# Kernel tuning notes

Measured on AMD Instinct MI355X. Metric: run time of the kernel, lower is better.

## Reference

```python
import jax, jax.numpy as jnp
import numpy as np

NEG_SLOPE = 0.2

def gat_conv(x, src, dst, n_nodes, W, a_src, a_dst, bias, heads, out_c):
    # x: [N, in]; W: [in, heads*out_c]; a_src/a_dst: [heads, out_c]; bias: [heads*out_c]
    h = (x @ W).reshape(n_nodes, heads, out_c)            # [N,H,C]
    e_s = jnp.sum(h * a_src, axis=-1)                     # [N,H] per-node src score
    e_d = jnp.sum(h * a_dst, axis=-1)                     # [N,H] per-node dst score
    e = jax.nn.leaky_relu(e_s[src] + e_d[dst], NEG_SLOPE) # [E,H]
    # segment softmax over destination neighborhoods
    emax = jax.ops.segment_max(e, dst, num_segments=n_nodes)  # [N,H]
    emax = jnp.where(jnp.isfinite(emax), emax, 0.0)
    p = jnp.exp(e - emax[dst])                            # [E,H]
    denom = jax.ops.segment_sum(p, dst, num_segments=n_nodes)  # [N,H]
    alpha = p / (denom[dst] + 1e-16)                      # [E,H]
    msg = h[src] * alpha[:, :, None]                      # [E,H,C]
    out = jax.ops.segment_sum(msg, dst, num_segments=n_nodes)  # [N,H,C]
    return out.reshape(n_nodes, heads * out_c) + bias


def setup_inputs() -> dict:
    key = jax.random.key(0)
    ks = jax.random.split(key, 10)
    N, E, IN, OUT, H = 50000, 1600000, 128, 32, 2
    x = jax.random.normal(ks[0], (N, IN), dtype=jnp.float32)
    edge_index = jax.random.randint(ks[1], (2, E), 0, N, dtype=jnp.int64)
    s = 0.1
    W1 = jax.random.normal(ks[2], (IN, H * OUT), dtype=jnp.float32) * s
    a_src1 = jax.random.normal(ks[3], (H, OUT), dtype=jnp.float32) * s
    a_dst1 = jax.random.normal(ks[4], (H, OUT), dtype=jnp.float32) * s
    b1 = jnp.zeros((H * OUT,), dtype=jnp.float32)
    W2 = jax.random.normal(ks[5], (H * OUT, OUT), dtype=jnp.float32) * s
    a_src2 = jax.random.normal(ks[6], (1, OUT), dtype=jnp.float32) * s
    a_dst2 = jax.random.normal(ks[7], (1, OUT), dtype=jnp.float32) * s
    b2 = jnp.zeros((OUT,), dtype=jnp.float32)
    return {"x": x, "edge_index": edge_index, "W1": W1, "a_src1": a_src1,
            "a_dst1": a_dst1, "b1": b1, "W2": W2, "a_src2": a_src2,
            "a_dst2": a_dst2, "b2": b2}


def reference(x, edge_index, W1, a_src1, a_dst1, b1, W2, a_src2, a_dst2, b2):
    N = x.shape[0]
    # add_self_loops=True (PyG GATConv default)
    loops = jnp.arange(N, dtype=edge_index.dtype)
    ei = jnp.concatenate([edge_index, jnp.stack([loops, loops])], axis=1)
    src, dst = ei[0], ei[1]
    h = gat_conv(x, src, dst, N, W1, a_src1, a_dst1, b1, heads=2, out_c=32)
    h = jax.nn.relu(h)
    out = gat_conv(h, src, dst, N, W2, a_src2, a_dst2, b2, heads=1, out_c=32)
    return out
```

## Files before the change

kernel.cpp:

```cpp
#include <hip/hip_runtime.h>
#include <hip/hip_fp16.h>

#define NEG_SLOPE 0.2f
#define DB 128
#define NB_MAX 512
#define EPB 4096
#define CAP 8192


__global__ __launch_bounds__(256) void k_part(const int* __restrict__ srcv,
                                              const int* __restrict__ dstv,
                                              int* __restrict__ gcur,
                                              int* __restrict__ ebuf, int E) {
  __shared__ int sh[NB_MAX];
  __shared__ int lbase[NB_MAX];
  int t = threadIdx.x;
  sh[t] = 0; sh[t + 256] = 0;
  __syncthreads();
  int base = blockIdx.x * EPB;
  int dd[16];
#pragma unroll
  for (int i = 0; i < 16; ++i) {
    int e = base + i * 256 + t;
    dd[i] = (e < E) ? dstv[e] : -1;
    if (dd[i] >= 0) atomicAdd(&sh[dd[i] >> 7], 1);
  }
  __syncthreads();
#pragma unroll
  for (int i = 0; i < 2; ++i) {
    int b = t + 256 * i;
    int c = sh[b];
    lbase[b] = c ? (b * CAP + atomicAdd(&gcur[b], c)) : 0;
    sh[b] = 0;
  }
  __syncthreads();
#pragma unroll
  for (int i = 0; i < 16; ++i) {
    if (dd[i] >= 0) {
      int e = base + i * 256 + t;
      int b = dd[i] >> 7;
      int r = atomicAdd(&sh[b], 1);
      ebuf[lbase[b] + r] = srcv[e] | ((dd[i] & 127) << 16);
    }
  }
}

__global__ __launch_bounds__(256) void k_csr(const int* __restrict__ gcur,
                                             const int* __restrict__ ebuf,
                                             int* __restrict__ rowbeg,
                                             int* __restrict__ rowend,
                                             int* __restrict__ col, int N) {
  int b = blockIdx.x;
  int cnt = gcur[b];
  int base = b * CAP;
  int dbase = b * DB;
  __shared__ int dh[DB];
  __shared__ int sc[DB];
  int t = threadIdx.x;
  if (t < DB) dh[t] = 0;
  __syncthreads();
  for (int j = t; j < cnt; j += 256) {
    int p = ebuf[base + j];
    atomicAdd(&dh[p >> 16], 1);
  }
  __syncthreads();
  int v = 0;
  if (t < DB) { v = dh[t]; sc[t] = v; }
  __syncthreads();
  for (int off = 1; off < DB; off <<= 1) {
    int u = 0;
    if (t < DB && t >= off) u = sc[t - off];
    __syncthreads();
    if (t < DB) sc[t] += u;
    __syncthreads();
  }
  if (t < DB) {
    int excl = sc[t] - v;
    int d = dbase + t;
    if (d < N) {
      rowbeg[d] = base + excl;
      rowend[d] = base + excl + v;
    }
    dh[t] = base + excl;
  }
  __syncthreads();
  for (int j = t; j < cnt; j += 256) {
    int p = ebuf[base + j];
    int r = atomicAdd(&dh[p >> 16], 1);
    col[r] = p & 0xFFFF;
  }
}

__global__ __launch_bounds__(256) void k_gemm1(const float* __restrict__ x,
                                               const float* __restrict__ W,
                                               const float* __restrict__ a_src,
                                               const float* __restrict__ a_dst,
                                               __half* __restrict__ h1,
                                               float* __restrict__ es,
                                               float* __restrict__ ed, int N) {
  __shared__ float sXT[128 * 64];
  __shared__ float sW[128 * 64];
  const int t = threadIdx.x;
  const int r0 = blockIdx.x * 64;

  {
    const float4* Wp = (const float4*)W;
    float4* sWp = (float4*)sW;
#pragma unroll
    for (int i = 0; i < 8; ++i) sWp[t + i * 256] = Wp[t + i * 256];
  }
  {
    int r = t & 63;
    int kq = t >> 6;
    int gr = r0 + r;
    bool ok = gr < N;
    const float* xr = x + (size_t)gr * 128;
#pragma unroll
    for (int p = 0; p < 8; ++p) {
      int k = (kq + p * 4) * 4;
      float4 v = ok ? *(const float4*)(xr + k) : make_float4(0.f, 0.f, 0.f, 0.f);
      sXT[(k + 0) * 64 + r] = v.x;
      sXT[(k + 1) * 64 + r] = v.y;
      sXT[(k + 2) * 64 + r] = v.z;
      sXT[(k + 3) * 64 + r] = v.w;
    }
  }
  __syncthreads();

  const int tx = t & 15, ty = t >> 4;
  float4 acc0 = make_float4(0.f, 0.f, 0.f, 0.f);
  float4 acc1 = acc0, acc2 = acc0, acc3 = acc0;
#pragma unroll 8
  for (int k = 0; k < 128; ++k) {
    float4 av = *(const float4*)(sXT + k * 64 + ty * 4);
    float4 bv = *(const float4*)(sW + k * 64 + tx * 4);
    acc0.x += av.x * bv.x; acc0.y += av.x * bv.y; acc0.z += av.x * bv.z; acc0.w += av.x * bv.w;
    acc1.x += av.y * bv.x; acc1.y += av.y * bv.y; acc1.z += av.y * bv.z; acc1.w += av.y * bv.w;
    acc2.x += av.z * bv.x; acc2.y += av.z * bv.y; acc2.z += av.z * bv.z; acc2.w += av.z * bv.w;
    acc3.x += av.w * bv.x; acc3.y += av.w * bv.y; acc3.z += av.w * bv.z; acc3.w += av.w * bv.w;
  }

  float4 accs[4] = {acc0, acc1, acc2, acc3};
#pragma unroll
  for (int i = 0; i < 4; ++i) {
    int gr = r0 + ty * 4 + i;
    if (gr < N) {
      union { __half2 h[2]; float2 f; } u;
      u.h[0] = __float22half2_rn(make_float2(accs[i].x, accs[i].y));
      u.h[1] = __float22half2_rn(make_float2(accs[i].z, accs[i].w));
      *(float2*)(h1 + (size_t)gr * 64 + tx * 4) = u.f;
    }
  }

  float4 asv = *(const float4*)(a_src + tx * 4);
  float4 adv = *(const float4*)(a_dst + tx * 4);
  float esp[4], edp[4];
#pragma unroll
  for (int i = 0; i < 4; ++i) {
    esp[i] = accs[i].x * asv.x + accs[i].y * asv.y + accs[i].z * asv.z + accs[i].w * asv.w;
    edp[i] = accs[i].x * adv.x + accs[i].y * adv.y + accs[i].z * adv.z + accs[i].w * adv.w;
  }
#pragma unroll
  for (int off = 1; off <= 4; off <<= 1) {
#pragma unroll
    for (int i = 0; i < 4; ++i) {
      esp[i] += __shfl_xor(esp[i], off);
      edp[i] += __shfl_xor(edp[i], off);
    }
  }
  if ((tx & 7) == 0) {
    int hh = tx >> 3;
#pragma unroll
    for (int i = 0; i < 4; ++i) {
      int gr = r0 + ty * 4 + i;
      if (gr < N) {
        es[gr * 2 + hh] = esp[i];
        ed[gr * 2 + hh] = edp[i];
      }
    }
  }
}

__global__ __launch_bounds__(256) void k_agg1(const int* __restrict__ rowbeg,
                                              const int* __restrict__ rowend,
                                              const int* __restrict__ col,
                                              const __half* __restrict__ h1,
                                              const float* __restrict__ es,
                                              const float* __restrict__ ed,
                                              const float* __restrict__ bias,
                                              float* __restrict__ out1, int N) {
  int d = (blockIdx.x * blockDim.x + threadIdx.x) >> 6;
  int lane = threadIdx.x & 63;
  if (d >= N) return;
  int g = lane >> 4;
  int q = lane & 15;
  int ch = q * 4;
  int hh = ch >> 5;
  float edv = ed[d * 2 + hh];

  float4 acc = make_float4(0.f, 0.f, 0.f, 0.f);
  float wsum = 0.f;

  if (g == 0) {
    float v = es[d * 2 + hh] + edv;
    v = v > 0.f ? v : NEG_SLOPE * v;
    float w = __expf(v);
    float2 raw = *(const float2*)(h1 + (size_t)d * 64 + ch);
    __half2* p2 = (__half2*)&raw;
    float2 lo = __half22float2(p2[0]);
    float2 hi = __half22float2(p2[1]);
    acc.x = w * lo.x; acc.y = w * lo.y; acc.z = w * hi.x; acc.w = w * hi.y;
    wsum = w;
  }

  int beg = rowbeg[d], end = rowend[d];
#pragma unroll 2
  for (int j = beg + g; j < end; j += 4) {
    int s = col[j];
    float vv = es[s * 2 + hh] + edv;
    vv = vv > 0.f ? vv : NEG_SLOPE * vv;
    float w = __expf(vv);
    float2 raw = *(const float2*)(h1 + (size_t)s * 64 + ch);
    __half2* p2 = (__half2*)&raw;
    float2 lo = __half22float2(p2[0]);
    float2 hi = __half22float2(p2[1]);
    acc.x += w * lo.x; acc.y += w * lo.y; acc.z += w * hi.x; acc.w += w * hi.y;
    wsum += w;
  }

#pragma unroll
  for (int off = 16; off <= 32; off <<= 1) {
    acc.x += __shfl_xor(acc.x, off);
    acc.y += __shfl_xor(acc.y, off);
    acc.z += __shfl_xor(acc.z, off);
    acc.w += __shfl_xor(acc.w, off);
    wsum  += __shfl_xor(wsum, off);
  }

  if (g == 0) {
    float inv = 1.f / (wsum + 1e-16f);
    const float4 bv = *(const float4*)(bias + ch);
    float4 o;
    o.x = acc.x * inv + bv.x;
    o.y = acc.y * inv + bv.y;
    o.z = acc.z * inv + bv.z;
    o.w = acc.w * inv + bv.w;
    *(float4*)(out1 + (size_t)d * 64 + ch) = o;
  }
}

__global__ __launch_bounds__(256) void k_gemm2(const float* __restrict__ out1,
                                               const float* __restrict__ W,
                                               const float* __restrict__ a_src,
                                               const float* __restrict__ a_dst,
                                               __half* __restrict__ hL2,
                                               float* __restrict__ es,
                                               float* __restrict__ ed, int N) {
  __shared__ float sXT[64 * 128];
  __shared__ float sW[64 * 32];
  const int t = threadIdx.x;
  const int r0 = blockIdx.x * 128;

  {
    const float4* Wp = (const float4*)W;
    float4* sWp = (float4*)sW;
#pragma unroll
    for (int i = 0; i < 2; ++i) sWp[t + i * 256] = Wp[t + i * 256];
  }
  {
    int r = t & 127;
    int kq = t >> 7;
    int gr = r0 + r;
    bool ok = gr < N;
    const float* xr = out1 + (size_t)gr * 64;
#pragma unroll
    for (int p = 0; p < 8; ++p) {
      int k = (kq + p * 2) * 4;
      float4 v = ok ? *(const float4*)(xr + k) : make_float4(0.f, 0.f, 0.f, 0.f);
      sXT[(k + 0) * 128 + r] = fmaxf(v.x, 0.f);
      sXT[(k + 1) * 128 + r] = fmaxf(v.y, 0.f);
      sXT[(k + 2) * 128 + r] = fmaxf(v.z, 0.f);
      sXT[(k + 3) * 128 + r] = fmaxf(v.w, 0.f);
    }
  }
  __syncthreads();

  const int tx = t & 7, ty = t >> 3;
  float4 acc0 = make_float4(0.f, 0.f, 0.f, 0.f);
  float4 acc1 = acc0, acc2 = acc0, acc3 = acc0;
#pragma unroll 8
  for (int k = 0; k < 64; ++k) {
    float4 av = *(const float4*)(sXT + k * 128 + ty * 4);
    float4 bv = *(const float4*)(sW + k * 32 + tx * 4);
    acc0.x += av.x * bv.x; acc0.y += av.x * bv.y; acc0.z += av.x * bv.z; acc0.w += av.x * bv.w;
    acc1.x += av.y * bv.x; acc1.y += av.y * bv.y; acc1.z += av.y * bv.z; acc1.w += av.y * bv.w;
    acc2.x += av.z * bv.x; acc2.y += av.z * bv.y; acc2.z += av.z * bv.z; acc2.w += av.z * bv.w;
    acc3.x += av.w * bv.x; acc3.y += av.w * bv.y; acc3.z += av.w * bv.z; acc3.w += av.w * bv.w;
  }

  float4 accs[4] = {acc0, acc1, acc2, acc3};
#pragma unroll
  for (int i = 0; i < 4; ++i) {
    int gr = r0 + ty * 4 + i;
    if (gr < N) {
      union { __half2 h[2]; float2 f; } u;
      u.h[0] = __float22half2_rn(make_float2(accs[i].x, accs[i].y));
      u.h[1] = __float22half2_rn(make_float2(accs[i].z, accs[i].w));
      *(float2*)(hL2 + (size_t)gr * 32 + tx * 4) = u.f;
    }
  }

  float4 asv = *(const float4*)(a_src + tx * 4);
  float4 adv = *(const float4*)(a_dst + tx * 4);
  float esp[4], edp[4];
#pragma unroll
  for (int i = 0; i < 4; ++i) {
    esp[i] = accs[i].x * asv.x + accs[i].y * asv.y + accs[i].z * asv.z + accs[i].w * asv.w;
    edp[i] = accs[i].x * adv.x + accs[i].y * adv.y + accs[i].z * adv.z + accs[i].w * adv.w;
  }
#pragma unroll
  for (int off = 1; off <= 4; off <<= 1) {
#pragma unroll
    for (int i = 0; i < 4; ++i) {
      esp[i] += __shfl_xor(esp[i], off);
      edp[i] += __shfl_xor(edp[i], off);
    }
  }
  if (tx == 0) {
#pragma unroll
    for (int i = 0; i < 4; ++i) {
      int gr = r0 + ty * 4 + i;
      if (gr < N) {
        es[gr] = esp[i];
        ed[gr] = edp[i];
      }
    }
  }
}

__global__ __launch_bounds__(256) void k_agg2(const int* __restrict__ rowbeg,
                                              const int* __restrict__ rowend,
                                              const int* __restrict__ col,
                                              const __half* __restrict__ hL2,
                                              const float* __restrict__ es,
                                              const float* __restrict__ ed,
                                              const float* __restrict__ bias,
                                              float* __restrict__ out, int N) {
  int d = (blockIdx.x * blockDim.x + threadIdx.x) >> 6;
  int lane = threadIdx.x & 63;
  if (d >= N) return;
  int g = lane >> 3;
  int q = lane & 7;
  int ch = q * 4;
  float edv = ed[d];

  float4 acc = make_float4(0.f, 0.f, 0.f, 0.f);
  float wsum = 0.f;

  if (g == 0) {
    float v = es[d] + edv;
    v = v > 0.f ? v : NEG_SLOPE * v;
    float w = __expf(v);
    float2 raw = *(const float2*)(hL2 + (size_t)d * 32 + ch);
    __half2* p2 = (__half2*)&raw;
    float2 lo = __half22float2(p2[0]);
    float2 hi = __half22float2(p2[1]);
    acc.x = w * lo.x; acc.y = w * lo.y; acc.z = w * hi.x; acc.w = w * hi.y;
    wsum = w;
  }

  int beg = rowbeg[d], end = rowend[d];
#pragma unroll 2
  for (int j = beg + g; j < end; j += 8) {
    int s = col[j];
    float vv = es[s] + edv;
    vv = vv > 0.f ? vv : NEG_SLOPE * vv;
    float w = __expf(vv);
    float2 raw = *(const float2*)(hL2 + (size_t)s * 32 + ch);
    __half2* p2 = (__half2*)&raw;
    float2 lo = __half22float2(p2[0]);
    float2 hi = __half22float2(p2[1]);
    acc.x += w * lo.x; acc.y += w * lo.y; acc.z += w * hi.x; acc.w += w * hi.y;
    wsum += w;
  }

#pragma unroll
  for (int off = 8; off <= 32; off <<= 1) {
    acc.x += __shfl_xor(acc.x, off);
    acc.y += __shfl_xor(acc.y, off);
    acc.z += __shfl_xor(acc.z, off);
    acc.w += __shfl_xor(acc.w, off);
    wsum  += __shfl_xor(wsum, off);
  }

  if (g == 0) {
    float inv = 1.f / (wsum + 1e-16f);
    const float4 bv = *(const float4*)(bias + ch);
    float4 o;
    o.x = acc.x * inv + bv.x;
    o.y = acc.y * inv + bv.y;
    o.z = acc.z * inv + bv.z;
    o.w = acc.w * inv + bv.w;
    *(float4*)(out + (size_t)d * 32 + ch) = o;
  }
}

extern "C" void kernel_launch(void* const* d_in, const int* in_sizes, int n_in,
                              void* d_out, int out_size, void* d_ws, size_t ws_size,
                              hipStream_t stream) {
  const float* x      = (const float*)d_in[0];
  const int*   ei     = (const int*)d_in[1];
  const float* W1     = (const float*)d_in[2];
  const float* a_src1 = (const float*)d_in[3];
  const float* a_dst1 = (const float*)d_in[4];
  const float* b1     = (const float*)d_in[5];
  const float* W2     = (const float*)d_in[6];
  const float* a_src2 = (const float*)d_in[7];
  const float* a_dst2 = (const float*)d_in[8];
  const float* b2     = (const float*)d_in[9];
  float* out = (float*)d_out;

  const int N = in_sizes[0] / 128;
  const int E = in_sizes[1] / 2;
  const int NB = (N + DB - 1) / DB;
  const int* srcv = ei;
  const int* dstv = ei + E;

  char* base = (char*)d_ws;
  size_t off = 0;
  auto carve = [&](size_t bytes) {
    void* p = base + off;
    off += (bytes + 15) & ~(size_t)15;
    return p;
  };
  __half* h1     = (__half*)carve((size_t)N * 64 * 2);
  float*  es1    = (float*)carve((size_t)N * 2 * 4);
  float*  ed1    = (float*)carve((size_t)N * 2 * 4);
  float*  out1   = (float*)carve((size_t)N * 64 * 4);
  __half* hL2    = (__half*)carve((size_t)N * 32 * 2);
  float*  es2    = (float*)carve((size_t)N * 4);
  float*  ed2    = (float*)carve((size_t)N * 4);
  int*    gcur   = (int*)carve((size_t)NB_MAX * 4);
  int*    rowbeg = (int*)carve((size_t)N * 4);
  int*    rowend = (int*)carve((size_t)N * 4);
  int*    col    = (int*)carve((size_t)NB * CAP * 4);
  int*    ebuf   = (int*)carve((size_t)NB * CAP * 4);

  const int pblocks = (E + EPB - 1) / EPB;

  hipMemsetAsync(gcur, 0, (size_t)NB_MAX * sizeof(int), stream);
  k_part<<<pblocks, 256, 0, stream>>>(srcv, dstv, gcur, ebuf, E);
  k_csr<<<NB, 256, 0, stream>>>(gcur, ebuf, rowbeg, rowend, col, N);

  k_gemm1<<<(N + 63) / 64, 256, 0, stream>>>(x, W1, a_src1, a_dst1, h1, es1, ed1, N);
  k_agg1<<<((size_t)N * 64 + 255) / 256, 256, 0, stream>>>(rowbeg, rowend, col, h1, es1, ed1, b1, out1, N);

  k_gemm2<<<(N + 127) / 128, 256, 0, stream>>>(out1, W2, a_src2, a_dst2, hL2, es2, ed2, N);
  k_agg2<<<((size_t)N * 64 + 255) / 256, 256, 0, stream>>>(rowbeg, rowend, col, hL2, es2, ed2, b2, out, N);
}
```

Before: 222.4 us.

## Merge GEMM1 with edge partition, use 16-bit CSR columns, widen aggregation loads

Folds the first-layer GEMM and the edge partition into one launch: the first G1 blocks do the GEMM and the rest partition edges, so the two independent jobs overlap and one launch is saved. The CSR column array becomes unsigned short, which halves the index traffic during aggregation. Both aggregation kernels now load 8 halves per lane (16-byte loads) with more edge groups per wavefront. The shared 64KB shared-memory block may lower occupancy for the partition blocks, and dropping the unroll pragma may reduce memory-level parallelism.

```diff
diff --git a/kernel.cpp b/kernel.cpp
--- a/kernel.cpp
+++ b/kernel.cpp
@@ -7,40 +7,125 @@
 #define EPB 4096
 #define CAP 8192
 
-
-__global__ __launch_bounds__(256) void k_part(const int* __restrict__ srcv,
-                                              const int* __restrict__ dstv,
-                                              int* __restrict__ gcur,
-                                              int* __restrict__ ebuf, int E) {
-  __shared__ int sh[NB_MAX];
-  __shared__ int lbase[NB_MAX];
-  int t = threadIdx.x;
-  sh[t] = 0; sh[t + 256] = 0;
-  __syncthreads();
-  int base = blockIdx.x * EPB;
-  int dd[16];
-#pragma unroll
-  for (int i = 0; i < 16; ++i) {
-    int e = base + i * 256 + t;
-    dd[i] = (e < E) ? dstv[e] : -1;
-    if (dd[i] >= 0) atomicAdd(&sh[dd[i] >> 7], 1);
-  }
-  __syncthreads();
-#pragma unroll
-  for (int i = 0; i < 2; ++i) {
-    int b = t + 256 * i;
-    int c = sh[b];
-    lbase[b] = c ? (b * CAP + atomicAdd(&gcur[b], c)) : 0;
-    sh[b] = 0;
-  }
-  __syncthreads();
-#pragma unroll
-  for (int i = 0; i < 16; ++i) {
-    if (dd[i] >= 0) {
+__global__ __launch_bounds__(256) void k_g1p(
+    const float* __restrict__ x, const float* __restrict__ W,
+    const float* __restrict__ a_src, const float* __restrict__ a_dst,
+    __half* __restrict__ h1, float* __restrict__ es, float* __restrict__ ed, int N,
+    const int* __restrict__ srcv, const int* __restrict__ dstv,
+    int* __restrict__ gcur, int* __restrict__ ebuf, int E, int G1) {
+  __shared__ __align__(16) char smem[65536];
+  const int t = threadIdx.x;
+
+  if ((int)blockIdx.x < G1) {
+    float* sXT = (float*)smem;
+    float* sW  = (float*)(smem + 32768);
+    const int r0 = blockIdx.x * 64;
+    {
+      const float4* Wp = (const float4*)W;
+      float4* sWp = (float4*)sW;
+#pragma unroll
+      for (int i = 0; i < 8; ++i) sWp[t + i * 256] = Wp[t + i * 256];
+    }
+    {
+      int r = t & 63;
+      int kq = t >> 6;
+      int gr = r0 + r;
+      bool ok = gr < N;
+      const float* xr = x + (size_t)gr * 128;
+#pragma unroll
+      for (int p = 0; p < 8; ++p) {
+        int k = (kq + p * 4) * 4;
+        float4 v = ok ? *(const float4*)(xr + k) : make_float4(0.f, 0.f, 0.f, 0.f);
+        sXT[(k + 0) * 64 + r] = v.x;
+        sXT[(k + 1) * 64 + r] = v.y;
+        sXT[(k + 2) * 64 + r] = v.z;
+        sXT[(k + 3) * 64 + r] = v.w;
+      }
+    }
+    __syncthreads();
+
+    const int tx = t & 15, ty = t >> 4;
+    float4 acc0 = make_float4(0.f, 0.f, 0.f, 0.f);
+    float4 acc1 = acc0, acc2 = acc0, acc3 = acc0;
+#pragma unroll 8
+    for (int k = 0; k < 128; ++k) {
+      float4 av = *(const float4*)(sXT + k * 64 + ty * 4);
+      float4 bv = *(const float4*)(sW + k * 64 + tx * 4);
+      acc0.x += av.x * bv.x; acc0.y += av.x * bv.y; acc0.z += av.x * bv.z; acc0.w += av.x * bv.w;
+      acc1.x += av.y * bv.x; acc1.y += av.y * bv.y; acc1.z += av.y * bv.z; acc1.w += av.y * bv.w;
+      acc2.x += av.z * bv.x; acc2.y += av.z * bv.y; acc2.z += av.z * bv.z; acc2.w += av.z * bv.w;
+      acc3.x += av.w * bv.x; acc3.y += av.w * bv.y; acc3.z += av.w * bv.z; acc3.w += av.w * bv.w;
+    }
+
+    float4 accs[4] = {acc0, acc1, acc2, acc3};
+#pragma unroll
+    for (int i = 0; i < 4; ++i) {
+      int gr = r0 + ty * 4 + i;
+      if (gr < N) {
+        union { __half2 h[2]; float2 f; } u;
+        u.h[0] = __float22half2_rn(make_float2(accs[i].x, accs[i].y));
+        u.h[1] = __float22half2_rn(make_float2(accs[i].z, accs[i].w));
+        *(float2*)(h1 + (size_t)gr * 64 + tx * 4) = u.f;
+      }
+    }
+
+    float4 asv = *(const float4*)(a_src + tx * 4);
+    float4 adv = *(const float4*)(a_dst + tx * 4);
+    float esp[4], edp[4];
+#pragma unroll
+    for (int i = 0; i < 4; ++i) {
+      esp[i] = accs[i].x * asv.x + accs[i].y * asv.y + accs[i].z * asv.z + accs[i].w * asv.w;
+      edp[i] = accs[i].x * adv.x + accs[i].y * adv.y + accs[i].z * adv.z + accs[i].w * adv.w;
+    }
+#pragma unroll
+    for (int off = 1; off <= 4; off <<= 1) {
+#pragma unroll
+      for (int i = 0; i < 4; ++i) {
+        esp[i] += __shfl_xor(esp[i], off);
+        edp[i] += __shfl_xor(edp[i], off);
+      }
+    }
+    if ((tx & 7) == 0) {
+      int hh = tx >> 3;
+#pragma unroll
+      for (int i = 0; i < 4; ++i) {
+        int gr = r0 + ty * 4 + i;
+        if (gr < N) {
+          es[gr * 2 + hh] = esp[i];
+          ed[gr * 2 + hh] = edp[i];
+        }
+      }
+    }
+  } else {
+    int* sh    = (int*)smem;
+    int* lbase = (int*)(smem + 2048);
+    sh[t] = 0; sh[t + 256] = 0;
+    __syncthreads();
+    int base = (blockIdx.x - G1) * EPB;
+    int dd[16];
+#pragma unroll
+    for (int i = 0; i < 16; ++i) {
       int e = base + i * 256 + t;
-      int b = dd[i] >> 7;
-      int r = atomicAdd(&sh[b], 1);
-      ebuf[lbase[b] + r] = srcv[e] | ((dd[i] & 127) << 16);
+      dd[i] = (e < E) ? dstv[e] : -1;
+      if (dd[i] >= 0) atomicAdd(&sh[dd[i] >> 7], 1);
+    }
+    __syncthreads();
+#pragma unroll
+    for (int i = 0; i < 2; ++i) {
+      int b = t + 256 * i;
+      int c = sh[b];
+      lbase[b] = c ? (b * CAP + atomicAdd(&gcur[b], c)) : 0;
+      sh[b] = 0;
+    }
+    __syncthreads();
+#pragma unroll
+    for (int i = 0; i < 16; ++i) {
+      if (dd[i] >= 0) {
+        int e = base + i * 256 + t;
+        int b = dd[i] >> 7;
+        int r = atomicAdd(&sh[b], 1);
+        ebuf[lbase[b] + r] = srcv[e] | ((dd[i] & 127) << 16);
+      }
     }
   }
 }
@@ -49,7 +134,7 @@
                                              const int* __restrict__ ebuf,
                                              int* __restrict__ rowbeg,
                                              int* __restrict__ rowend,
-                                             int* __restrict__ col, int N) {
+                                             unsigned short* __restrict__ col, int N) {
   int b = blockIdx.x;
   int cnt = gcur[b];
   int base = b * CAP;
@@ -87,103 +172,13 @@
   for (int j = t; j < cnt; j += 256) {
     int p = ebuf[base + j];
     int r = atomicAdd(&dh[p >> 16], 1);
-    col[r] = p & 0xFFFF;
-  }
-}
-
-__global__ __launch_bounds__(256) void k_gemm1(const float* __restrict__ x,
-                                               const float* __restrict__ W,
-                                               const float* __restrict__ a_src,
-                                               const float* __restrict__ a_dst,
-                                               __half* __restrict__ h1,
-                                               float* __restrict__ es,
-                                               float* __restrict__ ed, int N) {
-  __shared__ float sXT[128 * 64];
-  __shared__ float sW[128 * 64];
-  const int t = threadIdx.x;
-  const int r0 = blockIdx.x * 64;
-
-  {
-    const float4* Wp = (const float4*)W;
-    float4* sWp = (float4*)sW;
-#pragma unroll
-    for (int i = 0; i < 8; ++i) sWp[t + i * 256] = Wp[t + i * 256];
-  }
-  {
-    int r = t & 63;
-    int kq = t >> 6;
-    int gr = r0 + r;
-    bool ok = gr < N;
-    const float* xr = x + (size_t)gr * 128;
-#pragma unroll
-    for (int p = 0; p < 8; ++p) {
-      int k = (kq + p * 4) * 4;
-      float4 v = ok ? *(const float4*)(xr + k) : make_float4(0.f, 0.f, 0.f, 0.f);
-      sXT[(k + 0) * 64 + r] = v.x;
-      sXT[(k + 1) * 64 + r] = v.y;
-      sXT[(k + 2) * 64 + r] = v.z;
-      sXT[(k + 3) * 64 + r] = v.w;
-    }
-  }
-  __syncthreads();
-
-  const int tx = t & 15, ty = t >> 4;
-  float4 acc0 = make_float4(0.f, 0.f, 0.f, 0.f);
-  float4 acc1 = acc0, acc2 = acc0, acc3 = acc0;
-#pragma unroll 8
-  for (int k = 0; k < 128; ++k) {
-    float4 av = *(const float4*)(sXT + k * 64 + ty * 4);
-    float4 bv = *(const float4*)(sW + k * 64 + tx * 4);
-    acc0.x += av.x * bv.x; acc0.y += av.x * bv.y; acc0.z += av.x * bv.z; acc0.w += av.x * bv.w;
-    acc1.x += av.y * bv.x; acc1.y += av.y * bv.y; acc1.z += av.y * bv.z; acc1.w += av.y * bv.w;
-    acc2.x += av.z * bv.x; acc2.y += av.z * bv.y; acc2.z += av.z * bv.z; acc2.w += av.z * bv.w;
-    acc3.x += av.w * bv.x; acc3.y += av.w * bv.y; acc3.z += av.w * bv.z; acc3.w += av.w * bv.w;
-  }
-
-  float4 accs[4] = {acc0, acc1, acc2, acc3};
-#pragma unroll
-  for (int i = 0; i < 4; ++i) {
-    int gr = r0 + ty * 4 + i;
-    if (gr < N) {
-      union { __half2 h[2]; float2 f; } u;
-      u.h[0] = __float22half2_rn(make_float2(accs[i].x, accs[i].y));
-      u.h[1] = __float22half2_rn(make_float2(accs[i].z, accs[i].w));
-      *(float2*)(h1 + (size_t)gr * 64 + tx * 4) = u.f;
-    }
-  }
-
-  float4 asv = *(const float4*)(a_src + tx * 4);
-  float4 adv = *(const float4*)(a_dst + tx * 4);
-  float esp[4], edp[4];
-#pragma unroll
-  for (int i = 0; i < 4; ++i) {
-    esp[i] = accs[i].x * asv.x + accs[i].y * asv.y + accs[i].z * asv.z + accs[i].w * asv.w;
-    edp[i] = accs[i].x * adv.x + accs[i].y * adv.y + accs[i].z * adv.z + accs[i].w * adv.w;
-  }
-#pragma unroll
-  for (int off = 1; off <= 4; off <<= 1) {
-#pragma unroll
-    for (int i = 0; i < 4; ++i) {
-      esp[i] += __shfl_xor(esp[i], off);
-      edp[i] += __shfl_xor(edp[i], off);
-    }
-  }
-  if ((tx & 7) == 0) {
-    int hh = tx >> 3;
-#pragma unroll
-    for (int i = 0; i < 4; ++i) {
-      int gr = r0 + ty * 4 + i;
-      if (gr < N) {
-        es[gr * 2 + hh] = esp[i];
-        ed[gr * 2 + hh] = edp[i];
-      }
-    }
+    col[r] = (unsigned short)(p & 0xFFFF);
   }
 }
 
 __global__ __launch_bounds__(256) void k_agg1(const int* __restrict__ rowbeg,
                                               const int* __restrict__ rowend,
-                                              const int* __restrict__ col,
+                                              const unsigned short* __restrict__ col,
                                               const __half* __restrict__ h1,
                                               const float* __restrict__ es,
                                               const float* __restrict__ ed,
@@ -192,60 +187,63 @@
   int d = (blockIdx.x * blockDim.x + threadIdx.x) >> 6;
   int lane = threadIdx.x & 63;
   if (d >= N) return;
-  int g = lane >> 4;
-  int q = lane & 15;
-  int ch = q * 4;
-  int hh = ch >> 5;
+  int g = lane >> 3;
+  int q = lane & 7;
+  int ch = q * 8;
+  int hh = q >> 2;
   float edv = ed[d * 2 + hh];
 
-  float4 acc = make_float4(0.f, 0.f, 0.f, 0.f);
+  float a0 = 0.f, a1 = 0.f, a2 = 0.f, a3 = 0.f, a4 = 0.f, a5 = 0.f, a6 = 0.f, a7 = 0.f;
   float wsum = 0.f;
 
   if (g == 0) {
     float v = es[d * 2 + hh] + edv;
     v = v > 0.f ? v : NEG_SLOPE * v;
     float w = __expf(v);
-    float2 raw = *(const float2*)(h1 + (size_t)d * 64 + ch);
-    __half2* p2 = (__half2*)&raw;
-    float2 lo = __half22float2(p2[0]);
-    float2 hi = __half22float2(p2[1]);
-    acc.x = w * lo.x; acc.y = w * lo.y; acc.z = w * hi.x; acc.w = w * hi.y;
+    float4 raw = *(const float4*)(h1 + (size_t)d * 64 + ch);
+    const __half2* p2 = (const __half2*)&raw;
+    float2 f0 = __half22float2(p2[0]), f1 = __half22float2(p2[1]);
+    float2 f2 = __half22float2(p2[2]), f3 = __half22float2(p2[3]);
+    a0 = w * f0.x; a1 = w * f0.y; a2 = w * f1.x; a3 = w * f1.y;
+    a4 = w * f2.x; a5 = w * f2.y; a6 = w * f3.x; a7 = w * f3.y;
     wsum = w;
   }
 
   int beg = rowbeg[d], end = rowend[d];
-#pragma unroll 2
-  for (int j = beg + g; j < end; j += 4) {
+  for (int j = beg + g; j < end; j += 8) {
     int s = col[j];
     float vv = es[s * 2 + hh] + edv;
     vv = vv > 0.f ? vv : NEG_SLOPE * vv;
     float w = __expf(vv);
-    float2 raw = *(const float2*)(h1 + (size_t)s * 64 + ch);
-    __half2* p2 = (__half2*)&raw;
-    float2 lo = __half22float2(p2[0]);
-    float2 hi = __half22float2(p2[1]);
-    acc.x += w * lo.x; acc.y += w * lo.y; acc.z += w * hi.x; acc.w += w * hi.y;
+    float4 raw = *(const float4*)(h1 + (size_t)s * 64 + ch);
+    const __half2* p2 = (const __half2*)&raw;
+    float2 f0 = __half22float2(p2[0]), f1 = __half22float2(p2[1]);
+    float2 f2 = __half22float2(p2[2]), f3 = __half22float2(p2[3]);
+    a0 += w * f0.x; a1 += w * f0.y; a2 += w * f1.x; a3 += w * f1.y;
+    a4 += w * f2.x; a5 += w * f2.y; a6 += w * f3.x; a7 += w * f3.y;
     wsum += w;
   }
 
 #pragma unroll
-  for (int off = 16; off <= 32; off <<= 1) {
-    acc.x += __shfl_xor(acc.x, off);
-    acc.y += __shfl_xor(acc.y, off);
-    acc.z += __shfl_xor(acc.z, off);
-    acc.w += __shfl_xor(acc.w, off);
-    wsum  += __shfl_xor(wsum, off);
+  for (int off = 8; off <= 32; off <<= 1) {
+    a0 += __shfl_xor(a0, off); a1 += __shfl_xor(a1, off);
+    a2 += __shfl_xor(a2, off); a3 += __shfl_xor(a3, off);
+    a4 += __shfl_xor(a4, off); a5 += __shfl_xor(a5, off);
+    a6 += __shfl_xor(a6, off); a7 += __shfl_xor(a7, off);
+    wsum += __shfl_xor(wsum, off);
   }
 
   if (g == 0) {
     float inv = 1.f / (wsum + 1e-16f);
-    const float4 bv = *(const float4*)(bias + ch);
-    float4 o;
-    o.x = acc.x * inv + bv.x;
-    o.y = acc.y * inv + bv.y;
-    o.z = acc.z * inv + bv.z;
-    o.w = acc.w * inv + bv.w;
-    *(float4*)(out1 + (size_t)d * 64 + ch) = o;
+    const float4 bv0 = *(const float4*)(bias + ch);
+    const float4 bv1 = *(const float4*)(bias + ch + 4);
+    float4 o0, o1;
+    o0.x = a0 * inv + bv0.x; o0.y = a1 * inv + bv0.y;
+    o0.z = a2 * inv + bv0.z; o0.w = a3 * inv + bv0.w;
+    o1.x = a4 * inv + bv1.x; o1.y = a5 * inv + bv1.y;
+    o1.z = a6 * inv + bv1.z; o1.w = a7 * inv + bv1.w;
+    *(float4*)(out1 + (size_t)d * 64 + ch) = o0;
+    *(float4*)(out1 + (size_t)d * 64 + ch + 4) = o1;
   }
 }
 
@@ -340,7 +338,7 @@
 
 __global__ __launch_bounds__(256) void k_agg2(const int* __restrict__ rowbeg,
                                               const int* __restrict__ rowend,
-                                              const int* __restrict__ col,
+                                              const unsigned short* __restrict__ col,
                                               const __half* __restrict__ hL2,
                                               const float* __restrict__ es,
                                               const float* __restrict__ ed,
@@ -349,59 +347,62 @@
   int d = (blockIdx.x * blockDim.x + threadIdx.x) >> 6;
   int lane = threadIdx.x & 63;
   if (d >= N) return;
-  int g = lane >> 3;
-  int q = lane & 7;
-  int ch = q * 4;
+  int g = lane >> 2;
+  int q = lane & 3;
+  int ch = q * 8;
   float edv = ed[d];
 
-  float4 acc = make_float4(0.f, 0.f, 0.f, 0.f);
+  float a0 = 0.f, a1 = 0.f, a2 = 0.f, a3 = 0.f, a4 = 0.f, a5 = 0.f, a6 = 0.f, a7 = 0.f;
   float wsum = 0.f;
 
   if (g == 0) {
     float v = es[d] + edv;
     v = v > 0.f ? v : NEG_SLOPE * v;
     float w = __expf(v);
-    float2 raw = *(const float2*)(hL2 + (size_t)d * 32 + ch);
-    __half2* p2 = (__half2*)&raw;
-    float2 lo = __half22float2(p2[0]);
-    float2 hi = __half22float2(p2[1]);
-    acc.x = w * lo.x; acc.y = w * lo.y; acc.z = w * hi.x; acc.w = w * hi.y;
+    float4 raw = *(const float4*)(hL2 + (size_t)d * 32 + ch);
+    const __half2* p2 = (const __half2*)&raw;
+    float2 f0 = __half22float2(p2[0]), f1 = __half22float2(p2[1]);
+    float2 f2 = __half22float2(p2[2]), f3 = __half22float2(p2[3]);
+    a0 = w * f0.x; a1 = w * f0.y; a2 = w * f1.x; a3 = w * f1.y;
+    a4 = w * f2.x; a5 = w * f2.y; a6 = w * f3.x; a7 = w * f3.y;
     wsum = w;
   }
 
   int beg = rowbeg[d], end = rowend[d];
-#pragma unroll 2
-  for (int j = beg + g; j < end; j += 8) {
+  for (int j = beg + g; j < end; j += 16) {
     int s = col[j];
     float vv = es[s] + edv;
     vv = vv > 0.f ? vv : NEG_SLOPE * vv;
     float w = __expf(vv);
-    float2 raw = *(const float2*)(hL2 + (size_t)s * 32 + ch);
-    __half2* p2 = (__half2*)&raw;
-    float2 lo = __half22float2(p2[0]);
-    float2 hi = __half22float2(p2[1]);
-    acc.x += w * lo.x; acc.y += w * lo.y; acc.z += w * hi.x; acc.w += w * hi.y;
+    float4 raw = *(const float4*)(hL2 + (size_t)s * 32 + ch);
+    const __half2* p2 = (const __half2*)&raw;
+    float2 f0 = __half22float2(p2[0]), f1 = __half22float2(p2[1]);
+    float2 f2 = __half22float2(p2[2]), f3 = __half22float2(p2[3]);
+    a0 += w * f0.x; a1 += w * f0.y; a2 += w * f1.x; a3 += w * f1.y;
+    a4 += w * f2.x; a5 += w * f2.y; a6 += w * f3.x; a7 += w * f3.y;
     wsum += w;
   }
 
 #pragma unroll
-  for (int off = 8; off <= 32; off <<= 1) {
-    acc.x += __shfl_xor(acc.x, off);
-    acc.y += __shfl_xor(acc.y, off);
-    acc.z += __shfl_xor(acc.z, off);
-    acc.w += __shfl_xor(acc.w, off);
-    wsum  += __shfl_xor(wsum, off);
+  for (int off = 4; off <= 32; off <<= 1) {
+    a0 += __shfl_xor(a0, off); a1 += __shfl_xor(a1, off);
+    a2 += __shfl_xor(a2, off); a3 += __shfl_xor(a3, off);
+    a4 += __shfl_xor(a4, off); a5 += __shfl_xor(a5, off);
+    a6 += __shfl_xor(a6, off); a7 += __shfl_xor(a7, off);
+    wsum += __shfl_xor(wsum, off);
   }
 
   if (g == 0) {
     float inv = 1.f / (wsum + 1e-16f);
-    const float4 bv = *(const float4*)(bias + ch);
-    float4 o;
-    o.x = acc.x * inv + bv.x;
-    o.y = acc.y * inv + bv.y;
-    o.z = acc.z * inv + bv.z;
-    o.w = acc.w * inv + bv.w;
-    *(float4*)(out + (size_t)d * 32 + ch) = o;
+    const float4 bv0 = *(const float4*)(bias + ch);
+    const float4 bv1 = *(const float4*)(bias + ch + 4);
+    float4 o0, o1;
+    o0.x = a0 * inv + bv0.x; o0.y = a1 * inv + bv0.y;
+    o0.z = a2 * inv + bv0.z; o0.w = a3 * inv + bv0.w;
+    o1.x = a4 * inv + bv1.x; o1.y = a5 * inv + bv1.y;
+    o1.z = a6 * inv + bv1.z; o1.w = a7 * inv + bv1.w;
+    *(float4*)(out + (size_t)d * 32 + ch) = o0;
+    *(float4*)(out + (size_t)d * 32 + ch + 4) = o1;
   }
 }
 
@@ -443,16 +444,18 @@
   int*    gcur   = (int*)carve((size_t)NB_MAX * 4);
   int*    rowbeg = (int*)carve((size_t)N * 4);
   int*    rowend = (int*)carve((size_t)N * 4);
-  int*    col    = (int*)carve((size_t)NB * CAP * 4);
+  unsigned short* col = (unsigned short*)carve((size_t)NB * CAP * 2);
   int*    ebuf   = (int*)carve((size_t)NB * CAP * 4);
 
   const int pblocks = (E + EPB - 1) / EPB;
+  const int G1 = (N + 63) / 64;
 
   hipMemsetAsync(gcur, 0, (size_t)NB_MAX * sizeof(int), stream);
-  k_part<<<pblocks, 256, 0, stream>>>(srcv, dstv, gcur, ebuf, E);
+
+  k_g1p<<<G1 + pblocks, 256, 0, stream>>>(x, W1, a_src1, a_dst1, h1, es1, ed1, N,
+                                          srcv, dstv, gcur, ebuf, E, G1);
   k_csr<<<NB, 256, 0, stream>>>(gcur, ebuf, rowbeg, rowend, col, N);
 
-  k_gemm1<<<(N + 63) / 64, 256, 0, stream>>>(x, W1, a_src1, a_dst1, h1, es1, ed1, N);
   k_agg1<<<((size_t)N * 64 + 255) / 256, 256, 0, stream>>>(rowbeg, rowend, col, h1, es1, ed1, b1, out1, N);
 
   k_gemm2<<<(N + 127) / 128, 256, 0, stream>>>(out1, W2, a_src2, a_dst2, hL2, es2, ed2, N);
```

New measurement: 213.9 us. 3.8% less time.
